# Performance work log

Measured on AMD Instinct MI355X. Metric: run time of the kernel, lower is better.

Reference implementation:

```python
import jax, jax.numpy as jnp
import numpy as np

B = 4194304  # number of sequential rows


def setup_inputs() -> dict:
    key = jax.random.key(0)
    k1, k2, k3, k4 = jax.random.split(key, 4)
    x = jax.random.normal(k1, (B, 1, 3), dtype=jnp.float32)
    # nn.Linear(3, 3) params
    lim = 1.0 / np.sqrt(3.0)
    W = jax.random.uniform(k2, (3, 3), minval=-lim, maxval=lim, dtype=jnp.float32)
    b = jax.random.uniform(k3, (3,), minval=-lim, maxval=lim, dtype=jnp.float32)
    # FastNetwork init: (-1-1)*rand([3,1]) + 1  -> uniform in [-1, 1]
    net0 = jax.random.uniform(k4, (3, 1), minval=-1.0, maxval=1.0, dtype=jnp.float32)
    return {"x": x, "W": W, "b": b, "net0": net0}


def reference(x, W, b, net0):
    # x: [B,1,3]; W: [3,3]; b: [3]; net0: [3,1]
    xi = x[:, 0, :]                      # [B,3]
    # Updater: per-row Linear(3,3) -- batched as one matmul
    updates = xi @ W.T + b               # [B,3]

    def step(net, inp):
        x_row, u = inp                   # x_row: [3], u: [3]
        # 1/(1+exp(-10*(net + update - 0.5))) == sigmoid(10*(net + update - 0.5))
        net = jax.nn.sigmoid(10.0 * (net + u[:, None] - 0.5))  # [3,1]
        pred = x_row @ net               # [1]
        return net, pred

    _, preds = jax.lax.scan(step, net0, (xi, updates))
    return preds                         # [B,1]
```

## Files before the change

kernel.cpp:

```cpp
#include <hip/hip_runtime.h>


#if __has_builtin(__builtin_amdgcn_exp2f)
#define EXP2F(v) __builtin_amdgcn_exp2f(v)
#else
#define EXP2F(v) __expf(0.6931471805599453f * (v))
#endif

namespace {
constexpr int   BTOT   = 4194304;
constexpr int   CHUNK  = 32;
constexpr int   BLOCK  = 256;
constexpr int   BSTEPS = BLOCK * CHUNK;
constexpr int   WARM   = 32;
constexpr int   GRID   = BTOT / BSTEPS;
constexpr float KEXP   = -14.426950408889634f;
constexpr float EPS    = 1e-5f;
}

#define CVALS(X0_, X1_, X2_)                                                   \
  const float c0 = fmaf(kw00, (X0_), fmaf(kw01, (X1_), fmaf(kw02, (X2_), kb0))); \
  const float c1 = fmaf(kw10, (X0_), fmaf(kw11, (X1_), fmaf(kw12, (X2_), kb1))); \
  const float c2 = fmaf(kw20, (X0_), fmaf(kw21, (X1_), fmaf(kw22, (X2_), kb2)));

#define SIG(N, C) __builtin_amdgcn_rcpf(1.0f + EXP2F(fmaf(KEXP, (N), (C))))

#define PULL(VAL_) \
  __int_as_float(__builtin_amdgcn_ds_bpermute(a1, __float_as_int(VAL_)))

#define FETCH1(S_, XD0, XD1, XD2)                                              \
  XD0 = PULL(fx[3 * (S_) + 0]);                                                \
  XD1 = PULL(fx[3 * (S_) + 1]);                                                \
  XD2 = PULL(fx[3 * (S_) + 2]);                                                \
  if (lane == 0) {                                                             \
    const float4 wv_ = wb[(S_)];                                               \
    XD0 = wv_.x; XD1 = wv_.y; XD2 = wv_.z;                                     \
  }

#define DSTEP(X0_, X1_, X2_)                                                   \
  {                                                                            \
    CVALS(X0_, X1_, X2_)                                                       \
    lo0 = SIG(lo0, c0); hi0 = SIG(hi0, c0);                                    \
    lo1 = SIG(lo1, c1); hi1 = SIG(hi1, c1);                                    \
    lo2 = SIG(lo2, c2); hi2 = SIG(hi2, c2);                                    \
  }

#define SSTEP(X0_, X1_, X2_)                                                   \
  {                                                                            \
    CVALS(X0_, X1_, X2_)                                                       \
    m0 = SIG(m0, c0); m1 = SIG(m1, c1); m2 = SIG(m2, c2);                      \
  }

#define WBATCH(B_)                                                             \
  {                                                                            \
    float X00,X01,X02,X10,X11,X12,X20,X21,X22,X30,X31,X32;                     \
    FETCH1(4*(B_)+0, X00, X01, X02)                                            \
    FETCH1(4*(B_)+1, X10, X11, X12)                                            \
    FETCH1(4*(B_)+2, X20, X21, X22)                                            \
    FETCH1(4*(B_)+3, X30, X31, X32)                                            \
    if (!single) {                                                             \
      DSTEP(X00, X01, X02) DSTEP(X10, X11, X12)                                \
      DSTEP(X20, X21, X22) DSTEP(X30, X31, X32)                                \
      conv = ((hi0 - lo0) < EPS) & ((hi1 - lo1) < EPS) & ((hi2 - lo2) < EPS);  \
      if (__all(conv)) {                                                       \
        m0 = 0.5f * (lo0 + hi0); m1 = 0.5f * (lo1 + hi1);                      \
        m2 = 0.5f * (lo2 + hi2);                                               \
        single = true;                                                         \
      }                                                                        \
    } else {                                                                   \
      SSTEP(X00, X01, X02) SSTEP(X10, X11, X12)                                \
      SSTEP(X20, X21, X22) SSTEP(X30, X31, X32)                                \
    }                                                                          \
  }

#define MS(P_, X0_, X1_, X2_)                                                  \
  {                                                                            \
    CVALS(X0_, X1_, X2_)                                                       \
    m0 = SIG(m0, c0); m1 = SIG(m1, c1); m2 = SIG(m2, c2);                      \
    P_ = fmaf((X0_), m0, fmaf((X1_), m1, (X2_) * m2));                         \
  }

__global__ __launch_bounds__(BLOCK, 2) void Updater_65395172049297_kernel(
    const float* __restrict__ x, const float* __restrict__ W,
    const float* __restrict__ bv, const float* __restrict__ n0v,
    float* __restrict__ out)
{
    __shared__ float4 wbuf[BLOCK / 64][WARM];

    const float kw00 = KEXP * W[0], kw01 = KEXP * W[1], kw02 = KEXP * W[2];
    const float kw10 = KEXP * W[3], kw11 = KEXP * W[4], kw12 = KEXP * W[5];
    const float kw20 = KEXP * W[6], kw21 = KEXP * W[7], kw22 = KEXP * W[8];
    const float kb0 = KEXP * (bv[0] - 0.5f);
    const float kb1 = KEXP * (bv[1] - 0.5f);
    const float kb2 = KEXP * (bv[2] - 0.5f);
    const float n00 = n0v[0], n01 = n0v[1], n02 = n0v[2];

    const int  lane  = threadIdx.x & 63;
    const int  w     = threadIdx.x >> 6;
    const long S     = (long)blockIdx.x * BSTEPS;
    const long start = S + (long)threadIdx.x * CHUNK;
    const int  a1    = ((lane >= 1) ? (lane - 1) : 0) << 2;
    const float4* wb = wbuf[w];

    float4 wv;
    {
        const long wbase = S + (long)w * (64 * CHUNK);
        long sstep = wbase - WARM + lane;
        if (sstep < 0) sstep = 0;
        if (lane < WARM) {
            const float* xp = x + 3 * sstep;
            wv = make_float4(xp[0], xp[1], xp[2], 0.0f);
        }
    }

    float fx[96];
    {
        const float4* mp = reinterpret_cast<const float4*>(x + 3 * start);
#pragma unroll
        for (int i = 0; i < 24; ++i) {
            const float4 v = mp[i];
            fx[4 * i + 0] = v.x; fx[4 * i + 1] = v.y;
            fx[4 * i + 2] = v.z; fx[4 * i + 3] = v.w;
        }
    }

    if (lane < WARM) wbuf[w][lane] = wv;

    const bool exact = (start <= (long)WARM);
    float lo0, lo1, lo2, hi0, hi1, hi2;
    if (exact) { lo0 = hi0 = n00; lo1 = hi1 = n01; lo2 = hi2 = n02; }
    else       { lo0 = lo1 = lo2 = 0.0f; hi0 = hi1 = hi2 = 1.0f; }

    bool  conv = false, single = false;
    float m0 = n00, m1 = n01, m2 = n02;

    WBATCH(0) WBATCH(1) WBATCH(2) WBATCH(3)
    WBATCH(4) WBATCH(5) WBATCH(6) WBATCH(7)

    if (!single) {
        for (int at = 1; at < 10 && !conv; ++at) {
            long wl2 = (long)WARM << (2 * at);
            long bgn = start - wl2;
            bool ex2 = (bgn <= 0);
            if (ex2) bgn = 0;
            if (ex2) { lo0 = hi0 = n00; lo1 = hi1 = n01; lo2 = hi2 = n02; }
            else     { lo0 = lo1 = lo2 = 0.0f; hi0 = hi1 = hi2 = 1.0f; }
            const float4* bp = reinterpret_cast<const float4*>(x + 3 * bgn);
            const long ng = (start - bgn) >> 2;
            for (long q = 0; q < ng; ++q) {
                const float4 A4 = bp[3 * q], B4 = bp[3 * q + 1], C4 = bp[3 * q + 2];
                DSTEP(A4.x, A4.y, A4.z)
                DSTEP(A4.w, B4.x, B4.y)
                DSTEP(B4.z, B4.w, C4.x)
                DSTEP(C4.y, C4.z, C4.w)
            }
            conv = ex2 || (((hi0 - lo0) < EPS) & ((hi1 - lo1) < EPS) &
                           ((hi2 - lo2) < EPS));
        }
        m0 = 0.5f * (lo0 + hi0); m1 = 0.5f * (lo1 + hi1); m2 = 0.5f * (lo2 + hi2);
    }

    if (start == 0) { m0 = n00; m1 = n01; m2 = n02; }

    float4* op = reinterpret_cast<float4*>(out + start);
#pragma unroll
    for (int q = 0; q < 8; ++q) {
        float p0, p1, p2, p3;
        MS(p0, fx[12 * q + 0], fx[12 * q + 1],  fx[12 * q + 2]);
        MS(p1, fx[12 * q + 3], fx[12 * q + 4],  fx[12 * q + 5]);
        MS(p2, fx[12 * q + 6], fx[12 * q + 7],  fx[12 * q + 8]);
        MS(p3, fx[12 * q + 9], fx[12 * q + 10], fx[12 * q + 11]);
        op[q] = make_float4(p0, p1, p2, p3);
    }
}

extern "C" void kernel_launch(void* const* d_in, const int* in_sizes, int n_in,
                              void* d_out, int out_size, void* d_ws, size_t ws_size,
                              hipStream_t stream) {
    const float* x   = (const float*)d_in[0];
    const float* W   = (const float*)d_in[1];
    const float* bv  = (const float*)d_in[2];
    const float* n0v = (const float*)d_in[3];
    float*       out = (float*)d_out;
    Updater_65395172049297_kernel<<<GRID, BLOCK, 0, stream>>>(x, W, bv, n0v, out);
}
```

Before: 99.58 us.

## Stage per-thread input chunks through LDS for coalesced global loads

Replaces each thread's strided 24×float4 global reads of its own 32-step chunk with wave-cooperative coalesced float4 loads. The data is transposed through a double-buffered, padded LDS staging area, one quarter-wave at a time. The aim is to cut the uncoalesced memory traffic of the initial load. In exchange it adds about 12.8KB of LDS per block, which may lower occupancy, plus LDS round trips. It relies on wave-synchronous execution without barriers.

```diff
diff --git a/kernel.cpp b/kernel.cpp
--- a/kernel.cpp
+++ b/kernel.cpp
@@ -14,6 +14,7 @@
 constexpr int   BSTEPS = BLOCK * CHUNK;
 constexpr int   WARM   = 32;
 constexpr int   GRID   = BTOT / BSTEPS;
+constexpr int   QW     = 100;
 constexpr float KEXP   = -14.426950408889634f;
 constexpr float EPS    = 1e-5f;
 }
@@ -26,7 +27,7 @@
 #define SIG(N, C) __builtin_amdgcn_rcpf(1.0f + EXP2F(fmaf(KEXP, (N), (C))))
 
 #define PULL(VAL_) \
-  __int_as_float(__builtin_amdgcn_ds_bpermute(a1, __float_as_int(VAL_)))
+  __int_as_float(__builtin_amdgcn_ds_bpermute(pa1, __float_as_int(VAL_)))
 
 #define FETCH1(S_, XD0, XD1, XD2)                                              \
   XD0 = PULL(fx[3 * (S_) + 0]);                                                \
@@ -80,11 +81,28 @@
     P_ = fmaf((X0_), m0, fmaf((X1_), m1, (X2_) * m2));                         \
   }
 
+#define STW(P_, O_, V_) *reinterpret_cast<float4*>((P_) + (O_)) = (V_);
+#define RDQ(P_)                                                                \
+  _Pragma("unroll")                                                            \
+  for (int j = 0; j < 24; ++j) {                                               \
+    const float4 v = *reinterpret_cast<const float4*>((P_) + rb + 4 * j);      \
+    fx[4 * j + 0] = v.x; fx[4 * j + 1] = v.y;                                  \
+    fx[4 * j + 2] = v.z; fx[4 * j + 3] = v.w;                                  \
+  }
+#define LDQ(Q_, R0_, R1_, R2_, R3_, R4_, R5_)                                  \
+  R0_ = xw[384 * (Q_)       + lane]; R1_ = xw[384 * (Q_) +  64 + lane];        \
+  R2_ = xw[384 * (Q_) + 128 + lane]; R3_ = xw[384 * (Q_) + 192 + lane];        \
+  R4_ = xw[384 * (Q_) + 256 + lane]; R5_ = xw[384 * (Q_) + 320 + lane];
+#define WRQ(P_, R0_, R1_, R2_, R3_, R4_, R5_)                                  \
+  STW(P_, wa0, R0_) STW(P_, wa1, R1_) STW(P_, wa2, R2_)                        \
+  STW(P_, wa3, R3_) STW(P_, wa4, R4_) STW(P_, wa5, R5_)
+
 __global__ __launch_bounds__(BLOCK, 2) void Updater_65395172049297_kernel(
     const float* __restrict__ x, const float* __restrict__ W,
     const float* __restrict__ bv, const float* __restrict__ n0v,
     float* __restrict__ out)
 {
+    __shared__ float  qbuf[BLOCK / 64][2][16 * QW];
     __shared__ float4 wbuf[BLOCK / 64][WARM];
 
     const float kw00 = KEXP * W[0], kw01 = KEXP * W[1], kw02 = KEXP * W[2];
@@ -98,30 +116,49 @@
     const int  lane  = threadIdx.x & 63;
     const int  w     = threadIdx.x >> 6;
     const long S     = (long)blockIdx.x * BSTEPS;
-    const long start = S + (long)threadIdx.x * CHUNK;
-    const int  a1    = ((lane >= 1) ? (lane - 1) : 0) << 2;
+    const long Wb    = S + (long)w * (64 * CHUNK);
+    const long start = Wb + (long)lane * CHUNK;
+    const int  pa1   = ((lane >= 1) ? (lane - 1) : 0) << 2;
     const float4* wb = wbuf[w];
 
     float4 wv;
-    {
-        const long wbase = S + (long)w * (64 * CHUNK);
-        long sstep = wbase - WARM + lane;
+    if (lane < WARM) {
+        long sstep = Wb - WARM + lane;
         if (sstep < 0) sstep = 0;
-        if (lane < WARM) {
-            const float* xp = x + 3 * sstep;
-            wv = make_float4(xp[0], xp[1], xp[2], 0.0f);
-        }
-    }
+        const float* xp = x + 3 * sstep;
+        wv = make_float4(xp[0], xp[1], xp[2], 0.0f);
+    }
+
+    const float4* xw = reinterpret_cast<const float4*>(x) +
+                       ((long)blockIdx.x * 6144 + (long)w * 1536);
+    const int g0 = lane, g1 = 64 + lane, g2 = 128 + lane;
+    const int g3 = 192 + lane, g4 = 256 + lane, g5 = 320 + lane;
+    const int wa0 = (g0 / 24) * QW + (g0 % 24) * 4;
+    const int wa1 = (g1 / 24) * QW + (g1 % 24) * 4;
+    const int wa2 = (g2 / 24) * QW + (g2 % 24) * 4;
+    const int wa3 = (g3 / 24) * QW + (g3 % 24) * 4;
+    const int wa4 = (g4 / 24) * QW + (g4 % 24) * 4;
+    const int wa5 = (g5 / 24) * QW + (g5 % 24) * 4;
+    float* A  = qbuf[w][0];
+    float* Bf = qbuf[w][1];
+    const int myq = lane >> 4;
+    const int rb  = (lane & 15) * QW;
 
     float fx[96];
     {
-        const float4* mp = reinterpret_cast<const float4*>(x + 3 * start);
-#pragma unroll
-        for (int i = 0; i < 24; ++i) {
-            const float4 v = mp[i];
-            fx[4 * i + 0] = v.x; fx[4 * i + 1] = v.y;
-            fx[4 * i + 2] = v.z; fx[4 * i + 3] = v.w;
-        }
+        float4 r0, r1, r2, r3, r4, r5, s0, s1, s2, s3, s4, s5;
+        LDQ(0, r0, r1, r2, r3, r4, r5)
+        LDQ(1, s0, s1, s2, s3, s4, s5)
+        WRQ(A, r0, r1, r2, r3, r4, r5)
+        if (myq == 0) { RDQ(A) }
+        LDQ(2, r0, r1, r2, r3, r4, r5)
+        WRQ(Bf, s0, s1, s2, s3, s4, s5)
+        if (myq == 1) { RDQ(Bf) }
+        LDQ(3, s0, s1, s2, s3, s4, s5)
+        WRQ(A, r0, r1, r2, r3, r4, r5)
+        if (myq == 2) { RDQ(A) }
+        WRQ(Bf, s0, s1, s2, s3, s4, s5)
+        if (myq == 3) { RDQ(Bf) }
     }
 
     if (lane < WARM) wbuf[w][lane] = wv;
```

Result: no change. 101.0 us (+1.5%).
